# Kernel optimization log

Hardware: AMD Instinct MI355X
Metric: run time of the kernel (lower is better)

The kernel has to match this reference:

```python
import jax, jax.numpy as jnp
import numpy as np

IH, IW = 14, 14
NUM_HEADS = 16
HEAD_DIMS = 32
INP_DIMS = 512
B = 128


def make_relative_position_index(ih, iw):
    coords = np.stack(np.meshgrid(np.arange(ih), np.arange(iw), indexing='ij'))  # [2, ih, iw]
    cf = coords.reshape(2, -1)  # [2, n]
    rel = cf[:, :, None] - cf[:, None, :]  # [2, n, n]
    rel = rel.transpose(1, 2, 0)  # [n, n, 2]
    rel[:, :, 0] += ih - 1
    rel[:, :, 1] += iw - 1
    rel[:, :, 0] *= 2 * iw - 1
    return rel.sum(-1).astype(np.int64)  # [n, n]


def setup_inputs() -> dict:
    key = jax.random.key(0)
    k1, k2, k3, k4, k5 = jax.random.split(key, 5)
    n = IH * IW
    inner = NUM_HEADS * HEAD_DIMS
    x = jax.random.normal(k1, (B, n, INP_DIMS), dtype=jnp.float32)
    qkv_w = jax.random.normal(k2, (INP_DIMS, 3 * inner), dtype=jnp.float32) * 0.02
    rel_bias_table = jax.random.normal(k3, ((2 * IH - 1) * (2 * IW - 1), NUM_HEADS), dtype=jnp.float32) * 0.02
    proj_w = jax.random.normal(k4, (inner, INP_DIMS), dtype=jnp.float32) * 0.02
    proj_b = jax.random.normal(k5, (INP_DIMS,), dtype=jnp.float32) * 0.02
    rel_pos_index = jnp.asarray(make_relative_position_index(IH, IW))
    return {"x": x, "qkv_w": qkv_w, "rel_bias_table": rel_bias_table,
            "proj_w": proj_w, "proj_b": proj_b, "rel_pos_index": rel_pos_index}


def reference(x, qkv_w, rel_bias_table, proj_w, proj_b, rel_pos_index):
    b, n, c = x.shape
    h, hd = NUM_HEADS, HEAD_DIMS
    scale = (INP_DIMS // NUM_HEADS) ** (-0.5)
    qkv = x @ qkv_w  # [b, n, 3*h*hd]
    qkv = qkv.reshape(b, n, 3, h, hd).transpose(2, 0, 3, 1, 4)  # [3, b, h, n, hd]
    q, k, v = qkv[0] * scale, qkv[1], qkv[2]
    attn = jnp.einsum('bhqd,bhkd->bhqk', q, k)  # [b, h, n, n]
    # gather relative position bias: [n*n, h] -> [h, n, n]
    bias = rel_bias_table[rel_pos_index.reshape(-1)].reshape(n, n, h).transpose(2, 0, 1)
    attn = jax.nn.softmax(attn + bias[None], axis=-1)
    out = jnp.einsum('bhqk,bhkd->bhqd', attn, v)  # [b, h, n, hd]
    out = out.transpose(0, 2, 1, 3).reshape(b, n, h * hd)
    return out @ proj_w + proj_b
```

## Files before the change

kernel.cpp:

```cpp
#include <hip/hip_runtime.h>

#define NTOK 196
#define QPAD 208
#define KP 208
#define PSTR 232

typedef __attribute__((ext_vector_type(8))) short short8;
typedef __attribute__((ext_vector_type(4))) float float4_t;

__device__ __forceinline__ short f2bf(float f) {
  unsigned u = __float_as_uint(f);
  u = (u + 0x7fffu + ((u >> 16) & 1u)) >> 16;
  return (short)u;
}

__global__ __launch_bounds__(256) void fill_kernel(float* __restrict__ out,
                                                   int n) {
  int i = blockIdx.x * 256 + threadIdx.x;
  if (i < n) out[i] = 1000.0f;
}

__global__ __launch_bounds__(256) void cvt_kernel(const float* __restrict__ in,
                                                  short* __restrict__ out) {
  int i = (blockIdx.x * 256 + threadIdx.x) * 8;
  float4_t a = *(const float4_t*)&in[i];
  float4_t b = *(const float4_t*)&in[i + 4];
  short8 v;
  v[0] = f2bf(a[0]); v[1] = f2bf(a[1]); v[2] = f2bf(a[2]); v[3] = f2bf(a[3]);
  v[4] = f2bf(b[0]); v[5] = f2bf(b[1]); v[6] = f2bf(b[2]); v[7] = f2bf(b[3]);
  *(short8*)&out[i] = v;
}

__global__ __launch_bounds__(256) void transpose_kernel(
    const float* __restrict__ in, short* __restrict__ out, int R, int C) {
  __shared__ float tile[64][65];
  int c0 = blockIdx.x * 64, r0 = blockIdx.y * 64;
  int tc = threadIdx.x & 63, tr = threadIdx.x >> 6;
#pragma unroll
  for (int s = 0; s < 16; s++) {
    int r = s * 4 + tr;
    tile[r][tc] = in[(r0 + r) * C + c0 + tc];
  }
  __syncthreads();
#pragma unroll
  for (int s = 0; s < 16; s++) {
    int i = s * 4 + tr;
    out[(c0 + i) * R + r0 + tc] = f2bf(tile[tc][i]);
  }
}

__global__ __launch_bounds__(256) void bias_kernel(
    const float* __restrict__ table, const int* __restrict__ rpi,
    float* __restrict__ bias) {
  int idx = blockIdx.x * 256 + threadIdx.x;
  if (idx >= 16 * QPAD * KP) return;
  int h = idx / (QPAD * KP);
  int rem = idx % (QPAD * KP);
  int q = rem / KP, k = rem % KP;
  float v = 0.f;
  if (q < NTOK && k < NTOK) v = table[rpi[q * NTOK + k] * 16 + h];
  bias[idx] = v;
}

__device__ __forceinline__ void gemm_tile(const short* __restrict__ A,
                                          const short* __restrict__ B, int K,
                                          int m0, int n0, short (*As)[72],
                                          short (*Bs)[72], float4_t acc[4][4]) {
  int tid = threadIdx.x;
  int lane = tid & 63, wave = tid >> 6;
  int quad = lane >> 4, l16 = lane & 15;
  int wm = (wave >> 1) * 64, wn = (wave & 1) * 64;
  int srow = tid >> 3, scol = (tid & 7) * 8;
  for (int k0 = 0; k0 < K; k0 += 64) {
#pragma unroll
    for (int i = 0; i < 4; i++) {
      int r = srow + i * 32;
      *(short8*)&As[r][scol] = *(const short8*)&A[(m0 + r) * K + k0 + scol];
      *(short8*)&Bs[r][scol] = *(const short8*)&B[(n0 + r) * K + k0 + scol];
    }
    __syncthreads();
#pragma unroll
    for (int ks = 0; ks < 2; ks++) {
      short8 af[4], bfr[4];
#pragma unroll
      for (int i = 0; i < 4; i++) {
        af[i] = *(short8*)&As[wm + i * 16 + l16][ks * 32 + quad * 8];
        bfr[i] = *(short8*)&Bs[wn + i * 16 + l16][ks * 32 + quad * 8];
      }
#pragma unroll
      for (int mi = 0; mi < 4; mi++)
#pragma unroll
        for (int ni = 0; ni < 4; ni++)
          acc[mi][ni] = __builtin_amdgcn_mfma_f32_16x16x32_bf16(
              af[mi], bfr[ni], acc[mi][ni], 0, 0, 0);
    }
    __syncthreads();
  }
}

__global__ __launch_bounds__(256) void qkv_gemm(
    const short* __restrict__ xb, const short* __restrict__ wt1,
    short* __restrict__ qb, short* __restrict__ kb, short* __restrict__ vb) {
  __shared__ __align__(16) short As[128][72];
  __shared__ __align__(16) short Bs[128][72];
  float4_t acc[4][4];
  float4_t z = {0.f, 0.f, 0.f, 0.f};
#pragma unroll
  for (int i = 0; i < 4; i++)
#pragma unroll
    for (int j = 0; j < 4; j++) acc[i][j] = z;
  int m0 = blockIdx.y * 128, n0 = blockIdx.x * 128;
  gemm_tile(xb, wt1, 512, m0, n0, As, Bs, acc);
  int lane = threadIdx.x & 63, wave = threadIdx.x >> 6;
  int quad = lane >> 4, l16 = lane & 15;
  int wm = (wave >> 1) * 64, wn = (wave & 1) * 64;
  const float qscale = 0.17677669529663687f;
#pragma unroll
  for (int mi = 0; mi < 4; mi++)
#pragma unroll
    for (int ni = 0; ni < 4; ni++)
#pragma unroll
      for (int r = 0; r < 4; r++) {
        int rowg = m0 + wm + mi * 16 + quad * 4 + r;
        int colg = n0 + wn + ni * 16 + l16;
        float v = acc[mi][ni][r];
        int s = colg >> 9, rem = colg & 511;
        int h = rem >> 5, d = rem & 31;
        int b = rowg / NTOK, n = rowg - b * NTOK;
        int off = ((b * 16 + h) * QPAD + n) * 32 + d;
        if (s == 0)
          qb[off] = f2bf(v * qscale);
        else if (s == 1)
          kb[off] = f2bf(v);
        else
          vb[off] = f2bf(v);
      }
}

__global__ __launch_bounds__(256) void attn_kernel(
    const short* __restrict__ qb, const short* __restrict__ kb,
    const short* __restrict__ vb, const float* __restrict__ bias,
    short* __restrict__ aout) {
  __shared__ __align__(16) short vT[32][PSTR];
  __shared__ __align__(16) short P[4][16][PSTR];
  int bh = blockIdx.x, b = bh >> 4, h = bh & 15;
  int tid = threadIdx.x, wave = tid >> 6, lane = tid & 63;
  int quad = lane >> 4, l16 = lane & 15;
  int base_row = b * NTOK;
  const short* vsrc = vb + bh * QPAD * 32;
  for (int i = tid; i < NTOK * 32; i += 256) {
    int key = i >> 5, d = i & 31;
    vT[d][key] = vsrc[i];
  }
  for (int i = tid; i < 32 * (PSTR - NTOK); i += 256) {
    int d = i / (PSTR - NTOK), c = i - d * (PSTR - NTOK);
    vT[d][NTOK + c] = 0;
  }
  __syncthreads();
  float4_t z4 = {0.f, 0.f, 0.f, 0.f};
  for (int i2 = 0; i2 < 4; i2++) {
    bool active = (i2 < 3) || (wave == 0);
    int qt = (i2 < 3) ? (wave + 4 * i2) : 12;
    int qr0 = qt * 16;
    if (active) {
      short8 qf = *(const short8*)&qb[(bh * QPAD + qr0 + l16) * 32 + quad * 8];
      float4_t s[13];
#pragma unroll
      for (int kt = 0; kt < 13; kt++) {
        short8 kf =
            *(const short8*)&kb[(bh * QPAD + kt * 16 + l16) * 32 + quad * 8];
        s[kt] = __builtin_amdgcn_mfma_f32_16x16x32_bf16(qf, kf, z4, 0, 0, 0);
      }
      const float* brow = bias + (h * QPAD + qr0 + quad * 4) * KP;
#pragma unroll
      for (int kt = 0; kt < 13; kt++) {
        int col = kt * 16 + l16;
#pragma unroll
        for (int r = 0; r < 4; r++) s[kt][r] += brow[r * KP + col];
      }
      if (l16 >= 4) {
#pragma unroll
        for (int r = 0; r < 4; r++) s[12][r] = -1e30f;
      }
#pragma unroll
      for (int r = 0; r < 4; r++) {
        float m = s[0][r];
#pragma unroll
        for (int kt = 1; kt < 13; kt++) m = fmaxf(m, s[kt][r]);
        m = fmaxf(m, __shfl_xor(m, 8, 16));
        m = fmaxf(m, __shfl_xor(m, 4, 16));
        m = fmaxf(m, __shfl_xor(m, 2, 16));
        m = fmaxf(m, __shfl_xor(m, 1, 16));
        float sum = 0.f;
#pragma unroll
        for (int kt = 0; kt < 13; kt++) {
          float p = __expf(s[kt][r] - m);
          s[kt][r] = p;
          sum += p;
        }
        sum += __shfl_xor(sum, 8, 16);
        sum += __shfl_xor(sum, 4, 16);
        sum += __shfl_xor(sum, 2, 16);
        sum += __shfl_xor(sum, 1, 16);
        float inv = 1.f / sum;
        short* prow = &P[wave][quad * 4 + r][0];
#pragma unroll
        for (int kt = 0; kt < 13; kt++)
          prow[kt * 16 + l16] = f2bf(s[kt][r] * inv);
        prow[208 + l16] = 0;
      }
    }
    __syncthreads();
    if (active) {
      float4_t o0 = z4, o1 = z4;
#pragma unroll
      for (int kt = 0; kt < 7; kt++) {
        short8 pf = *(short8*)&P[wave][l16][kt * 32 + quad * 8];
        short8 vf0 = *(short8*)&vT[l16][kt * 32 + quad * 8];
        short8 vf1 = *(short8*)&vT[16 + l16][kt * 32 + quad * 8];
        o0 = __builtin_amdgcn_mfma_f32_16x16x32_bf16(pf, vf0, o0, 0, 0, 0);
        o1 = __builtin_amdgcn_mfma_f32_16x16x32_bf16(pf, vf1, o1, 0, 0, 0);
      }
#pragma unroll
      for (int r = 0; r < 4; r++) {
        int row = qr0 + quad * 4 + r;
        if (row < NTOK) {
          int off = (base_row + row) * 512 + h * 32;
          aout[off + l16] = f2bf(o0[r]);
          aout[off + 16 + l16] = f2bf(o1[r]);
        }
      }
    }
    __syncthreads();
  }
}

__global__ __launch_bounds__(256, 2) void fused_attn(
    const short* __restrict__ xb, const short* __restrict__ wt1,
    const float* __restrict__ bias, short* __restrict__ aout) {
  __shared__ __align__(16) short R1[64 * PSTR];
  __shared__ __align__(16) short R2[32 * PSTR];
  __shared__ __align__(16) short Qs[224][40];
  __shared__ __align__(16) short Ks[224][40];
  short(*As)[40] = (short(*)[40])R1;
  short(*P)[PSTR] = (short(*)[PSTR])R1;
  short(*Bs)[40] = (short(*)[40])R2;
  short(*vTs)[PSTR] = (short(*)[PSTR])R2;

  int bh = blockIdx.x, b = bh >> 4, h = bh & 15;
  int tid = threadIdx.x, wave = tid >> 6, lane = tid & 63;
  int quad = lane >> 4, l16 = lane & 15;
  int base_row = b * NTOK;

  float4_t z4 = {0.f, 0.f, 0.f, 0.f};
  float4_t acc[4][6];
#pragma unroll
  for (int i = 0; i < 4; i++)
#pragma unroll
    for (int n = 0; n < 6; n++) acc[i][n] = z4;

  int srow = tid >> 2, scol = (tid & 3) * 8;
  for (int k0 = 0; k0 < 512; k0 += 32) {
#pragma unroll
    for (int i = 0; i < 4; i++) {
      int r = srow + i * 64;
      if (r < 224) {
        int gr = base_row + r;
        if (gr > 25087) gr = 25087;
        *(short8*)&As[r][scol] = *(const short8*)&xb[gr * 512 + k0 + scol];
      }
    }
#pragma unroll
    for (int i = 0; i < 2; i++) {
      int r = srow + i * 64;
      if (r < 96) {
        int sec = r >> 5, r32 = r & 31;
        *(short8*)&Bs[r][scol] =
            *(const short8*)&wt1[(sec * 512 + h * 32 + r32) * 512 + k0 + scol];
      }
    }
    __syncthreads();
    short8 af[4], bfv[6];
#pragma unroll
    for (int i = 0; i < 4; i++) {
      int mt = (i < 3) ? (wave + 4 * i) : (12 + (wave & 1));
      af[i] = *(short8*)&As[mt * 16 + l16][quad * 8];
    }
#pragma unroll
    for (int n = 0; n < 6; n++) bfv[n] = *(short8*)&Bs[n * 16 + l16][quad * 8];
#pragma unroll
    for (int i = 0; i < 4; i++)
#pragma unroll
      for (int n = 0; n < 6; n++)
        acc[i][n] = __builtin_amdgcn_mfma_f32_16x16x32_bf16(af[i], bfv[n],
                                                            acc[i][n], 0, 0, 0);
    __syncthreads();
  }
  const float qscale = 0.17677669529663687f;
#pragma unroll
  for (int i = 0; i < 4; i++) {
    if (i == 3 && wave >= 2) break;
    int mt = (i < 3) ? (wave + 4 * i) : (12 + wave);
    int row0 = mt * 16 + quad * 4;
#pragma unroll
    for (int n = 0; n < 6; n++) {
      int c = n * 16 + l16;
#pragma unroll
      for (int r = 0; r < 4; r++) {
        int row = row0 + r;
        float v = acc[i][n][r];
        if (c < 32)
          Qs[row][c] = f2bf(v * qscale);
        else if (c < 64)
          Ks[row][c - 32] = f2bf(v);
        else
          vTs[c - 64][row] = f2bf(v);
      }
    }
  }
  __syncthreads();
  for (int i2 = 0; i2 < 4; i2++) {
    bool active = (i2 < 3) || (wave == 0);
    int qt = (i2 < 3) ? (wave + 4 * i2) : 12;
    int qr0 = qt * 16;
    if (active) {
      short8 qf = *(short8*)&Qs[qr0 + l16][quad * 8];
      float4_t s[13];
#pragma unroll
      for (int kt = 0; kt < 13; kt++) {
        short8 kf = *(short8*)&Ks[kt * 16 + l16][quad * 8];
        s[kt] = __builtin_amdgcn_mfma_f32_16x16x32_bf16(qf, kf, z4, 0, 0, 0);
      }
      const float* brow = bias + (h * QPAD + qr0 + quad * 4) * KP;
#pragma unroll
      for (int kt = 0; kt < 13; kt++) {
        int col = kt * 16 + l16;
#pragma unroll
        for (int r = 0; r < 4; r++) s[kt][r] += brow[r * KP + col];
      }
      if (l16 >= 4) {
#pragma unroll
        for (int r = 0; r < 4; r++) s[12][r] = -1e30f;
      }
      int prow_base = wave * 16 + quad * 4;
#pragma unroll
      for (int r = 0; r < 4; r++) {
        float m = s[0][r];
#pragma unroll
        for (int kt = 1; kt < 13; kt++) m = fmaxf(m, s[kt][r]);
        m = fmaxf(m, __shfl_xor(m, 8, 16));
        m = fmaxf(m, __shfl_xor(m, 4, 16));
        m = fmaxf(m, __shfl_xor(m, 2, 16));
        m = fmaxf(m, __shfl_xor(m, 1, 16));
        float sum = 0.f;
#pragma unroll
        for (int kt = 0; kt < 13; kt++) {
          float p = __expf(s[kt][r] - m);
          s[kt][r] = p;
          sum += p;
        }
        sum += __shfl_xor(sum, 8, 16);
        sum += __shfl_xor(sum, 4, 16);
        sum += __shfl_xor(sum, 2, 16);
        sum += __shfl_xor(sum, 1, 16);
        float inv = 1.f / sum;
        short* prow = &P[prow_base + r][0];
#pragma unroll
        for (int kt = 0; kt < 13; kt++)
          prow[kt * 16 + l16] = f2bf(s[kt][r] * inv);
        prow[208 + l16] = 0;
      }
    }
    __syncthreads();
    if (active) {
      float4_t o0 = z4, o1 = z4;
#pragma unroll
      for (int kt = 0; kt < 7; kt++) {
        short8 pf = *(short8*)&P[wave * 16 + l16][kt * 32 + quad * 8];
        short8 vf0 = *(short8*)&vTs[l16][kt * 32 + quad * 8];
        short8 vf1 = *(short8*)&vTs[16 + l16][kt * 32 + quad * 8];
        o0 = __builtin_amdgcn_mfma_f32_16x16x32_bf16(pf, vf0, o0, 0, 0, 0);
        o1 = __builtin_amdgcn_mfma_f32_16x16x32_bf16(pf, vf1, o1, 0, 0, 0);
      }
#pragma unroll
      for (int r = 0; r < 4; r++) {
        int row = qr0 + quad * 4 + r;
        if (row < NTOK) {
          int off = (base_row + row) * 512 + h * 32;
          aout[off + l16] = f2bf(o0[r]);
          aout[off + 16 + l16] = f2bf(o1[r]);
        }
      }
    }
    __syncthreads();
  }
}

__global__ __launch_bounds__(256) void proj_gemm(
    const short* __restrict__ a, const short* __restrict__ wt,
    const float* __restrict__ pb, float* __restrict__ out) {
  __shared__ __align__(16) short As[128][72];
  __shared__ __align__(16) short Bs[128][72];
  float4_t acc[4][4];
  float4_t z = {0.f, 0.f, 0.f, 0.f};
#pragma unroll
  for (int i = 0; i < 4; i++)
#pragma unroll
    for (int j = 0; j < 4; j++) acc[i][j] = z;
  int m0 = blockIdx.y * 128, n0 = blockIdx.x * 128;
  gemm_tile(a, wt, 512, m0, n0, As, Bs, acc);
  int lane = threadIdx.x & 63, wave = threadIdx.x >> 6;
  int quad = lane >> 4, l16 = lane & 15;
  int wm = (wave >> 1) * 64, wn = (wave & 1) * 64;
#pragma unroll
  for (int mi = 0; mi < 4; mi++)
#pragma unroll
    for (int ni = 0; ni < 4; ni++) {
      int colg = n0 + wn + ni * 16 + l16;
      float bv = pb[colg];
#pragma unroll
      for (int r = 0; r < 4; r++) {
        int rowg = m0 + wm + mi * 16 + quad * 4 + r;
        out[rowg * 512 + colg] = acc[mi][ni][r] + bv;
      }
    }
}

extern "C" void kernel_launch(void* const* d_in, const int* in_sizes, int n_in,
                              void* d_out, int out_size, void* d_ws,
                              size_t ws_size, hipStream_t stream) {
  const float* x = (const float*)d_in[0];
  const float* qkv_w = (const float*)d_in[1];
  const float* table = (const float*)d_in[2];
  const float* proj_w = (const float*)d_in[3];
  const float* proj_b = (const float*)d_in[4];
  const int* rpi = (const int*)d_in[5];
  float* out = (float*)d_out;

  char* w = (char*)d_ws;
  short* wt1 = (short*)(w);
  short* wt2 = (short*)(w + 1572864);
  float* bias = (float*)(w + 2097152);
  short* xb = (short*)(w + 4866048);
  short* qb = (short*)(w + 30556160);
  short* kb = (short*)(w + 57819136);
  short* vb = (short*)(w + 85082112);
  const size_t NEEDED_SPLIT = 112345088;
  const size_t NEEDED_FUSED = 30556160 + 25690112;

  transpose_kernel<<<dim3(24, 8), 256, 0, stream>>>(qkv_w, wt1, 512, 1536);
  transpose_kernel<<<dim3(8, 8), 256, 0, stream>>>(proj_w, wt2, 512, 512);
  bias_kernel<<<(16 * QPAD * KP + 255) / 256, 256, 0, stream>>>(table, rpi,
                                                                bias);
  if (ws_size >= NEEDED_SPLIT) {
    short* aout = xb;
    cvt_kernel<<<25088 * 512 / (256 * 8), 256, 0, stream>>>(x, xb);
    qkv_gemm<<<dim3(12, 196), 256, 0, stream>>>(xb, wt1, qb, kb, vb);
    attn_kernel<<<2048, 256, 0, stream>>>(qb, kb, vb, bias, aout);
    proj_gemm<<<dim3(4, 196), 256, 0, stream>>>(aout, wt2, proj_b, out);
  } else if (ws_size >= NEEDED_FUSED) {
    short* aout = (short*)(w + 30556160);
    cvt_kernel<<<25088 * 512 / (256 * 8), 256, 0, stream>>>(x, xb);
    fused_attn<<<2048, 256, 0, stream>>>(xb, wt1, bias, aout);
    proj_gemm<<<dim3(4, 196), 256, 0, stream>>>(aout, wt2, proj_b, out);
  } else {
    fill_kernel<<<(out_size + 255) / 256, 256, 0, stream>>>(out, out_size);
  }
}
```

Before: 281.3 us.

## Store V transposed from QKV GEMM, drop LDS transpose; swizzle GEMM blocks across XCDs

The QKV GEMM epilogue now writes V directly in a [d][key] transposed layout with packed 4-wide stores, and a small kernel zero-pads the tail keys. The attention kernel then reads V fragments straight from global memory instead of staging a transposed copy in LDS, which removes the scalar transpose loop and two block-wide barriers per iteration. Both GEMMs remap block indices so that consecutive tiles land on the same XCD, aiming for better L2 reuse. The costs are an extra launch and V fragment reads that go to global/L2 rather than LDS.

Measured after the change: 372.7 us. 32.5% more time.

```diff
diff --git a/kernel.cpp b/kernel.cpp
--- a/kernel.cpp
+++ b/kernel.cpp
@@ -4,8 +4,10 @@
 #define QPAD 208
 #define KP 208
 #define PSTR 232
+#define VKP 208
 
 typedef __attribute__((ext_vector_type(8))) short short8;
+typedef __attribute__((ext_vector_type(4))) short short4_t;
 typedef __attribute__((ext_vector_type(4))) float float4_t;
 
 __device__ __forceinline__ short f2bf(float f) {
@@ -62,6 +64,14 @@
   bias[idx] = v;
 }
 
+__global__ __launch_bounds__(256) void vpad_kernel(short* __restrict__ vb) {
+  int i = blockIdx.x * 256 + threadIdx.x;
+  if (i >= 2048 * 32 * 3) return;
+  int row = i / 3, g = i - 3 * (i / 3);
+  short4_t z = {0, 0, 0, 0};
+  *(short4_t*)&vb[row * VKP + 196 + g * 4] = z;
+}
+
 __device__ __forceinline__ void gemm_tile(const short* __restrict__ A,
                                           const short* __restrict__ B, int K,
                                           int m0, int n0, short (*As)[72],
@@ -109,7 +119,11 @@
   for (int i = 0; i < 4; i++)
 #pragma unroll
     for (int j = 0; j < 4; j++) acc[i][j] = z;
-  int m0 = blockIdx.y * 128, n0 = blockIdx.x * 128;
+  int lin = blockIdx.x + blockIdx.y * 12;
+  int xcd = lin & 7, loc = lin >> 3;
+  int nl = xcd * 294 + loc;
+  int bx = nl % 12, by = nl / 12;
+  int m0 = by * 128, n0 = bx * 128;
   gemm_tile(xb, wt1, 512, m0, n0, As, Bs, acc);
   int lane = threadIdx.x & 63, wave = threadIdx.x >> 6;
   int quad = lane >> 4, l16 = lane & 15;
@@ -118,120 +132,121 @@
 #pragma unroll
   for (int mi = 0; mi < 4; mi++)
 #pragma unroll
-    for (int ni = 0; ni < 4; ni++)
-#pragma unroll
-      for (int r = 0; r < 4; r++) {
-        int rowg = m0 + wm + mi * 16 + quad * 4 + r;
-        int colg = n0 + wn + ni * 16 + l16;
-        float v = acc[mi][ni][r];
-        int s = colg >> 9, rem = colg & 511;
-        int h = rem >> 5, d = rem & 31;
-        int b = rowg / NTOK, n = rowg - b * NTOK;
-        int off = ((b * 16 + h) * QPAD + n) * 32 + d;
-        if (s == 0)
-          qb[off] = f2bf(v * qscale);
-        else if (s == 1)
-          kb[off] = f2bf(v);
-        else
-          vb[off] = f2bf(v);
-      }
+    for (int ni = 0; ni < 4; ni++) {
+      int colg = n0 + wn + ni * 16 + l16;
+      int s = colg >> 9, rem = colg & 511;
+      int h = rem >> 5, d = rem & 31;
+      int rowg0 = m0 + wm + mi * 16 + quad * 4;
+      if (s == 2) {
+        int b = rowg0 / NTOK, nt = rowg0 - b * NTOK;
+        short4_t v4;
+        v4[0] = f2bf(acc[mi][ni][0]);
+        v4[1] = f2bf(acc[mi][ni][1]);
+        v4[2] = f2bf(acc[mi][ni][2]);
+        v4[3] = f2bf(acc[mi][ni][3]);
+        *(short4_t*)&vb[((b * 16 + h) * 32 + d) * VKP + nt] = v4;
+      } else {
+#pragma unroll
+        for (int r = 0; r < 4; r++) {
+          int rowg = rowg0 + r;
+          int b = rowg / NTOK, n = rowg - b * NTOK;
+          int off = ((b * 16 + h) * QPAD + n) * 32 + d;
+          if (s == 0)
+            qb[off] = f2bf(acc[mi][ni][r] * qscale);
+          else
+            kb[off] = f2bf(acc[mi][ni][r]);
+        }
+      }
+    }
 }
 
 __global__ __launch_bounds__(256) void attn_kernel(
     const short* __restrict__ qb, const short* __restrict__ kb,
     const short* __restrict__ vb, const float* __restrict__ bias,
     short* __restrict__ aout) {
-  __shared__ __align__(16) short vT[32][PSTR];
   __shared__ __align__(16) short P[4][16][PSTR];
   int bh = blockIdx.x, b = bh >> 4, h = bh & 15;
   int tid = threadIdx.x, wave = tid >> 6, lane = tid & 63;
   int quad = lane >> 4, l16 = lane & 15;
   int base_row = b * NTOK;
-  const short* vsrc = vb + bh * QPAD * 32;
-  for (int i = tid; i < NTOK * 32; i += 256) {
-    int key = i >> 5, d = i & 31;
-    vT[d][key] = vsrc[i];
-  }
-  for (int i = tid; i < 32 * (PSTR - NTOK); i += 256) {
-    int d = i / (PSTR - NTOK), c = i - d * (PSTR - NTOK);
-    vT[d][NTOK + c] = 0;
-  }
-  __syncthreads();
+  const short* vbase = vb + bh * 32 * VKP;
   float4_t z4 = {0.f, 0.f, 0.f, 0.f};
+  short8 z8 = {0, 0, 0, 0, 0, 0, 0, 0};
   for (int i2 = 0; i2 < 4; i2++) {
     bool active = (i2 < 3) || (wave == 0);
+    if (!active) break;
     int qt = (i2 < 3) ? (wave + 4 * i2) : 12;
     int qr0 = qt * 16;
-    if (active) {
-      short8 qf = *(const short8*)&qb[(bh * QPAD + qr0 + l16) * 32 + quad * 8];
-      float4_t s[13];
+    short8 qf = *(const short8*)&qb[(bh * QPAD + qr0 + l16) * 32 + quad * 8];
+    float4_t s[13];
+#pragma unroll
+    for (int kt = 0; kt < 13; kt++) {
+      short8 kf =
+          *(const short8*)&kb[(bh * QPAD + kt * 16 + l16) * 32 + quad * 8];
+      s[kt] = __builtin_amdgcn_mfma_f32_16x16x32_bf16(qf, kf, z4, 0, 0, 0);
+    }
+    const float* brow = bias + (h * QPAD + qr0 + quad * 4) * KP;
+#pragma unroll
+    for (int kt = 0; kt < 13; kt++) {
+      int col = kt * 16 + l16;
+#pragma unroll
+      for (int r = 0; r < 4; r++) s[kt][r] += brow[r * KP + col];
+    }
+    if (l16 >= 4) {
+#pragma unroll
+      for (int r = 0; r < 4; r++) s[12][r] = -1e30f;
+    }
+#pragma unroll
+    for (int r = 0; r < 4; r++) {
+      float m = s[0][r];
+#pragma unroll
+      for (int kt = 1; kt < 13; kt++) m = fmaxf(m, s[kt][r]);
+      m = fmaxf(m, __shfl_xor(m, 8, 16));
+      m = fmaxf(m, __shfl_xor(m, 4, 16));
+      m = fmaxf(m, __shfl_xor(m, 2, 16));
+      m = fmaxf(m, __shfl_xor(m, 1, 16));
+      float sum = 0.f;
 #pragma unroll
       for (int kt = 0; kt < 13; kt++) {
-        short8 kf =
-            *(const short8*)&kb[(bh * QPAD + kt * 16 + l16) * 32 + quad * 8];
-        s[kt] = __builtin_amdgcn_mfma_f32_16x16x32_bf16(qf, kf, z4, 0, 0, 0);
-      }
-      const float* brow = bias + (h * QPAD + qr0 + quad * 4) * KP;
-#pragma unroll
-      for (int kt = 0; kt < 13; kt++) {
-        int col = kt * 16 + l16;
-#pragma unroll
-        for (int r = 0; r < 4; r++) s[kt][r] += brow[r * KP + col];
-      }
-      if (l16 >= 4) {
-#pragma unroll
-        for (int r = 0; r < 4; r++) s[12][r] = -1e30f;
-      }
-#pragma unroll
-      for (int r = 0; r < 4; r++) {
-        float m = s[0][r];
-#pragma unroll
-        for (int kt = 1; kt < 13; kt++) m = fmaxf(m, s[kt][r]);
-        m = fmaxf(m, __shfl_xor(m, 8, 16));
-        m = fmaxf(m, __shfl_xor(m, 4, 16));
-        m = fmaxf(m, __shfl_xor(m, 2, 16));
-        m = fmaxf(m, __shfl_xor(m, 1, 16));
-        float sum = 0.f;
-#pragma unroll
-        for (int kt = 0; kt < 13; kt++) {
-          float p = __expf(s[kt][r] - m);
-          s[kt][r] = p;
-          sum += p;
-        }
-        sum += __shfl_xor(sum, 8, 16);
-        sum += __shfl_xor(sum, 4, 16);
-        sum += __shfl_xor(sum, 2, 16);
-        sum += __shfl_xor(sum, 1, 16);
-        float inv = 1.f / sum;
-        short* prow = &P[wave][quad * 4 + r][0];
-#pragma unroll
-        for (int kt = 0; kt < 13; kt++)
-          prow[kt * 16 + l16] = f2bf(s[kt][r] * inv);
-        prow[208 + l16] = 0;
-      }
-    }
-    __syncthreads();
-    if (active) {
-      float4_t o0 = z4, o1 = z4;
-#pragma unroll
-      for (int kt = 0; kt < 7; kt++) {
-        short8 pf = *(short8*)&P[wave][l16][kt * 32 + quad * 8];
-        short8 vf0 = *(short8*)&vT[l16][kt * 32 + quad * 8];
-        short8 vf1 = *(short8*)&vT[16 + l16][kt * 32 + quad * 8];
-        o0 = __builtin_amdgcn_mfma_f32_16x16x32_bf16(pf, vf0, o0, 0, 0, 0);
-        o1 = __builtin_amdgcn_mfma_f32_16x16x32_bf16(pf, vf1, o1, 0, 0, 0);
-      }
-#pragma unroll
-      for (int r = 0; r < 4; r++) {
-        int row = qr0 + quad * 4 + r;
-        if (row < NTOK) {
-          int off = (base_row + row) * 512 + h * 32;
-          aout[off + l16] = f2bf(o0[r]);
-          aout[off + 16 + l16] = f2bf(o1[r]);
-        }
-      }
-    }
-    __syncthreads();
+        float p = __expf(s[kt][r] - m);
+        s[kt][r] = p;
+        sum += p;
+      }
+      sum += __shfl_xor(sum, 8, 16);
+      sum += __shfl_xor(sum, 4, 16);
+      sum += __shfl_xor(sum, 2, 16);
+      sum += __shfl_xor(sum, 1, 16);
+      float inv = 1.f / sum;
+      short* prow = &P[wave][quad * 4 + r][0];
+#pragma unroll
+      for (int kt = 0; kt < 13; kt++)
+        prow[kt * 16 + l16] = f2bf(s[kt][r] * inv);
+      prow[208 + l16] = 0;
+    }
+    float4_t o0 = z4, o1 = z4;
+#pragma unroll
+    for (int kt = 0; kt < 7; kt++) {
+      short8 pf = *(short8*)&P[wave][l16][kt * 32 + quad * 8];
+      short8 vf0, vf1;
+      if (kt < 6 || quad < 2) {
+        vf0 = *(const short8*)&vbase[l16 * VKP + kt * 32 + quad * 8];
+        vf1 = *(const short8*)&vbase[(16 + l16) * VKP + kt * 32 + quad * 8];
+      } else {
+        vf0 = z8;
+        vf1 = z8;
+      }
+      o0 = __builtin_amdgcn_mfma_f32_16x16x32_bf16(pf, vf0, o0, 0, 0, 0);
+      o1 = __builtin_amdgcn_mfma_f32_16x16x32_bf16(pf, vf1, o1, 0, 0, 0);
+    }
+#pragma unroll
+    for (int r = 0; r < 4; r++) {
+      int row = qr0 + quad * 4 + r;
+      if (row < NTOK) {
+        int off = (base_row + row) * 512 + h * 32;
+        aout[off + l16] = f2bf(o0[r]);
+        aout[off + 16 + l16] = f2bf(o1[r]);
+      }
+    }
   }
 }
 
@@ -407,7 +422,11 @@
   for (int i = 0; i < 4; i++)
 #pragma unroll
     for (int j = 0; j < 4; j++) acc[i][j] = z;
-  int m0 = blockIdx.y * 128, n0 = blockIdx.x * 128;
+  int lin = blockIdx.x + blockIdx.y * 4;
+  int xcd = lin & 7, loc = lin >> 3;
+  int nl = xcd * 98 + loc;
+  int bx = nl % 4, by = nl / 4;
+  int m0 = by * 128, n0 = bx * 128;
   gemm_tile(a, wt, 512, m0, n0, As, Bs, acc);
   int lane = threadIdx.x & 63, wave = threadIdx.x >> 6;
   int quad = lane >> 4, l16 = lane & 15;
@@ -454,6 +473,7 @@
                                                                 bias);
   if (ws_size >= NEEDED_SPLIT) {
     short* aout = xb;
+    vpad_kernel<<<(2048 * 32 * 3 + 255) / 256, 256, 0, stream>>>(vb);
     cvt_kernel<<<25088 * 512 / (256 * 8), 256, 0, stream>>>(x, xb);
     qkv_gemm<<<dim3(12, 196), 256, 0, stream>>>(xb, wt1, qb, kb, vb);
     attn_kernel<<<2048, 256, 0, stream>>>(qb, kb, vb, bias, aout);
```
